# Optimization experiments

Measured on AMD Instinct MI355X. Metric: run time of the kernel, lower is better.

## Reference

```python
import jax, jax.numpy as jnp
from jax import lax
import numpy as np

B, L, FEAT, EXTRA, K1 = 128, 128, 36, 12, 3
EMB, H, A, T_OUT = 6, 1024, 256, 24
CONV_OUT = FEAT - 2 * (K1 - 1)  # 32


def _conv1d(x, w):
    return lax.conv_general_dilated(x, w, (1,), 'VALID', dimension_numbers=('NCW', 'OIW', 'NCW'))


def _lstm(x_t, h, c, Wih, Whh, b):
    g = x_t @ Wih.T + h @ Whh.T + b
    i, f, gg, o = jnp.split(g, 4, axis=-1)
    c = jax.nn.sigmoid(f) * c + jax.nn.sigmoid(i) * jnp.tanh(gg)
    h = jax.nn.sigmoid(o) * jnp.tanh(c)
    return h, c


def setup_inputs():
    key = jax.random.key(0)
    ks = jax.random.split(key, 20)
    s = 0.05
    r = lambda k, sh: jax.random.normal(k, sh, jnp.float32) * s
    return {
        'x': jax.random.normal(ks[0], (B, L, FEAT + EXTRA), jnp.float32),
        'conv1_w': r(ks[1], (L, L, K1)), 'conv1_b': r(ks[2], (L,)),
        'conv2_w': r(ks[3], (L, L, K1)), 'conv2_b': r(ks[4], (L,)),
        'lin3_w': r(ks[5], (EMB, CONV_OUT)), 'lin3_b': r(ks[6], (EMB,)),
        'enc_Wih': r(ks[7], (4 * H, EMB + EXTRA)), 'enc_Whh': r(ks[8], (4 * H, H)), 'enc_b': r(ks[9], (4 * H,)),
        'attn_Wq': r(ks[10], (A, H)), 'attn_Wk': r(ks[11], (A, H)), 'attn_Wv': r(ks[12], (1, A)),
        'dec_Wih': r(ks[13], (4 * H, 2 * H)), 'dec_Whh': r(ks[14], (4 * H, H)), 'dec_b': r(ks[15], (4 * H,)),
        'out_w': r(ks[16], (1, H)), 'out_b': r(ks[17], (1,)),
    }


def reference(x, conv1_w, conv1_b, conv2_w, conv2_b, lin3_w, lin3_b,
              enc_Wih, enc_Whh, enc_b, attn_Wq, attn_Wk, attn_Wv,
              dec_Wih, dec_Whh, dec_b, out_w, out_b):
    # CNN feature extractor over the dense (short-interval) features
    dense = x[:, :, :FEAT]                                   # (B, L, 36)
    h1 = jax.nn.softplus(_conv1d(dense, conv1_w) + conv1_b[None, :, None])
    h2 = jax.nn.relu(_conv1d(h1, conv2_w) + conv2_b[None, :, None])  # (B, L, 32)
    lin = jnp.einsum('blf,ef->ble', h2, lin3_w) + lin3_b     # (B, L, EMB)
    lstm_in = jnp.concatenate([lin, x[:, :, FEAT:]], axis=2)  # (B, L, EMB+EXTRA)

    # LSTM encoder
    def enc_step(carry, xt):
        h, c = carry
        h, c = _lstm(xt, h, c, enc_Wih, enc_Whh, enc_b)
        return (h, c), h
    z = jnp.zeros((B, H), jnp.float32)
    (h, c), outs = lax.scan(enc_step, (z, z), lstm_in.transpose(1, 0, 2))
    enc_out = outs.transpose(1, 0, 2)                        # (B, L, H)
    s = enc_out[:, -1]

    # fixed-size key buffer; original appends s_t each step (lengths 128..151)
    M = L - 1 + T_OUT
    buf0 = jnp.zeros((B, M, H), jnp.float32).at[:, :L - 1].set(enc_out[:, :-1])
    pos = jnp.arange(M)

    def dec_step(carry, t):
        h, c, s, buf = carry
        buf = lax.dynamic_update_slice(buf, s[:, None, :], (0, L - 1 + t, 0))
        mask = (pos <= L - 1 + t).astype(buf.dtype)
        q = jnp.stack([h, c], axis=1)                        # (B, 2, H)
        qp = q @ attn_Wq.T                                   # (B, 2, A)
        kp = buf @ attn_Wk.T                                 # (B, M, A)
        feats = jnp.tanh(qp[:, :, None, :] + kp[:, None, :, :])  # (B, 2, M, A)
        scores = jnp.einsum('bnma,a->bnm', feats, attn_Wv[0])
        # original: softmax over dim=1 (query axis); mask keys post-softmax
        w = jax.nn.softmax(scores, axis=1) * mask[None, None, :]
        ctx = jnp.einsum('bnm,bmh->bnh', w, buf).reshape(B, 2 * H)
        h, c = _lstm(ctx, h, c, dec_Wih, dec_Whh, dec_b)
        y = (h @ out_w.T + out_b)[:, 0]
        return (h, c, h, buf), y

    _, ys = lax.scan(dec_step, (h, c, s, buf0), jnp.arange(T_OUT))
    return ys.T                                              # (B, T_OUT)
```

## Files before the change

### kernel.cpp

```cpp
#include <hip/hip_runtime.h>
#include <math.h>


#define NB 128
#define NL 128
#define NH 1024
#define NA 256
#define NT 24
#define NM 151
#define ENCB 128

typedef __attribute__((ext_vector_type(8))) short bf16x8;
typedef __attribute__((ext_vector_type(8))) short s16x8;
typedef __attribute__((ext_vector_type(4))) float f32x4;

#define MFMA(a, b, acc) __builtin_amdgcn_mfma_f32_16x16x32_bf16(a, b, acc, 0, 0, 0)

#define I16_SCALE 32767.0f
#define I16_INV   (1.0f / 32767.0f)

__device__ __forceinline__ float sig_f(float x) {
  return 1.0f / (1.0f + __expf(-x));
}
__device__ __forceinline__ float tanh_f(float x) {
  x = fminf(9.0f, fmaxf(-9.0f, x));
  float e = __expf(2.0f * x);
  return (e - 1.0f) / (e + 1.0f);
}
__device__ __forceinline__ unsigned short f2bf(float f) {
  unsigned int u = __float_as_uint(f);
  u = (u + 0x7FFFu + ((u >> 16) & 1u)) >> 16;
  return (unsigned short)u;
}
__device__ __forceinline__ float bf2f(unsigned short u) {
  return __uint_as_float(((unsigned int)u) << 16);
}
__device__ __forceinline__ short f2i16(float f) {
  return (short)__float2int_rn(f * I16_SCALE);
}

__device__ __forceinline__ void ast8(unsigned short* p, unsigned short a,
                                     unsigned short b, unsigned short cc,
                                     unsigned short d) {
  unsigned long long u = (unsigned long long)a | ((unsigned long long)b << 16) |
                         ((unsigned long long)cc << 32) |
                         ((unsigned long long)d << 48);
  __hip_atomic_store((unsigned long long*)p, u, __ATOMIC_RELAXED,
                     __HIP_MEMORY_SCOPE_AGENT);
}

#define LLCLD(dst, ptr) \
  asm volatile("global_load_dwordx4 %0, %1, off sc0 sc1" \
               : "=v"(dst) : "v"(ptr))

#define WAITC(n)                                              \
  asm volatile("s_waitcnt vmcnt(" #n ")" ::: "memory");       \
  __builtin_amdgcn_sched_barrier(0)

__device__ __forceinline__ void gbar(unsigned int* bar, int t) {
  __syncthreads();
  if (threadIdx.x == 0) {
    unsigned int* cnt = bar + t * 32;
    __hip_atomic_fetch_add(cnt, 1u, __ATOMIC_RELAXED,
                           __HIP_MEMORY_SCOPE_AGENT);
    while (__hip_atomic_load(cnt, __ATOMIC_RELAXED,
                             __HIP_MEMORY_SCOPE_AGENT) < (unsigned)ENCB)
      __builtin_amdgcn_s_sleep(2);
  }
  __syncthreads();
}

__global__ __launch_bounds__(128) void conv_front(
    const float* __restrict__ x,
    const float* __restrict__ w1, const float* __restrict__ b1,
    const float* __restrict__ w2, const float* __restrict__ b2,
    const float* __restrict__ w3, const float* __restrict__ b3,
    float* __restrict__ lstm_in)
{
  int b = blockIdx.x;
  int t = threadIdx.x;
  __shared__ float d[128][36];
  __shared__ float h1[128][34];
  __shared__ float h2[128][32];

  const float* xr = x + (size_t)(b * NL + t) * 48;
  #pragma unroll
  for (int f = 0; f < 36; ++f) d[t][f] = xr[f];
  __syncthreads();

  float acc[34];
  {
    float bias = b1[t];
    #pragma unroll
    for (int w = 0; w < 34; ++w) acc[w] = bias;
  }
  const float* wr = w1 + t * 384;
  for (int ci = 0; ci < 128; ++ci) {
    float row[36];
    #pragma unroll
    for (int f = 0; f < 36; ++f) row[f] = d[ci][f];
    float wa = wr[ci * 3 + 0], wb = wr[ci * 3 + 1], wc = wr[ci * 3 + 2];
    #pragma unroll
    for (int w = 0; w < 34; ++w)
      acc[w] += row[w] * wa + row[w + 1] * wb + row[w + 2] * wc;
  }
  #pragma unroll
  for (int w = 0; w < 34; ++w) {
    float z = acc[w];
    h1[t][w] = (z > 20.0f) ? z : log1pf(__expf(z));
  }
  __syncthreads();

  float acc2[32];
  {
    float bias = b2[t];
    #pragma unroll
    for (int w = 0; w < 32; ++w) acc2[w] = bias;
  }
  const float* wr2 = w2 + t * 384;
// ... 87 lines not shown
  int t2 = o >> 6;
  int l15 = lane & 15, q = lane >> 4;
  int grow = (l15 >> 2) * 1024 + t2 * 4 + (l15 & 3);
  unsigned short hv[8], lv[8];
  #pragma unroll
  for (int j = 0; j < 8; ++j) {
    int k = q * 8 + j;
    float v = (k < 18) ? wih[(size_t)grow * 18 + k] : 0.0f;
    hv[j] = f2bf(v);
    lv[j] = f2bf(v - bf2f(hv[j]));
  }
  size_t e = (size_t)o * 8;
  *(ushort4*)(hi + e) = make_ushort4(hv[0], hv[1], hv[2], hv[3]);
  *(ushort4*)(hi + e + 4) = make_ushort4(hv[4], hv[5], hv[6], hv[7]);
  *(ushort4*)(lo + e) = make_ushort4(lv[0], lv[1], lv[2], lv[3]);
  *(ushort4*)(lo + e + 4) = make_ushort4(lv[4], lv[5], lv[6], lv[7]);
}

__global__ void frag_xs(const float* __restrict__ lstm_in,
                        unsigned short* __restrict__ hi,
                        unsigned short* __restrict__ lo)
{
  int o = blockIdx.x * 256 + threadIdx.x;
  if (o >= 65536) return;
  int lane = o & 63;
  int btile = (o >> 6) & 7;
  int t = o >> 9;
  int l15 = lane & 15, q = lane >> 4;
  int b = btile * 16 + l15;
  unsigned short hv[8], lv[8];
  #pragma unroll
  for (int j = 0; j < 8; ++j) {
    int k = q * 8 + j;
    float v = (k < 18) ? lstm_in[(size_t)(b * NL + t) * 18 + k] : 0.0f;
    hv[j] = f2bf(v);
    lv[j] = f2bf(v - bf2f(hv[j]));
  }
  size_t e = (size_t)o * 8;
  *(ushort4*)(hi + e) = make_ushort4(hv[0], hv[1], hv[2], hv[3]);
  *(ushort4*)(hi + e + 4) = make_ushort4(hv[4], hv[5], hv[6], hv[7]);
  *(ushort4*)(lo + e) = make_ushort4(lv[0], lv[1], lv[2], lv[3]);
  *(ushort4*)(lo + e + 4) = make_ushort4(lv[4], lv[5], lv[6], lv[7]);
}

__global__ void init_all(float* __restrict__ c,
                         unsigned short* __restrict__ hhi0,
                         unsigned short* __restrict__ hlo0,
                         float* __restrict__ out,
                         unsigned int* __restrict__ bar) {
  int i = blockIdx.x * 256 + threadIdx.x;
  if (i < NB * NH) { c[i] = 0.0f; hhi0[i] = 0; hlo0[i] = 0; }
  if (i < NB * NT) out[i] = 0.0f;
  if (i < 8192) bar[i] = 0;
}

__global__ __launch_bounds__(512) void enc_all(
    unsigned short* __restrict__ hfA_hi, unsigned short* __restrict__ hfA_lo,
    unsigned short* __restrict__ hfB_hi, unsigned short* __restrict__ hfB_lo,
    const unsigned short* __restrict__ Wf_hi,
    const unsigned short* __restrict__ Wf_lo,
    const unsigned short* __restrict__ Wxf_hi,
    const unsigned short* __restrict__ Wxf_lo,
    const unsigned short* __restrict__ xsf_hi,
    const unsigned short* __restrict__ xsf_lo,
    const float* __restrict__ encb,
    float* __restrict__ c,
    short* __restrict__ buf,
    unsigned int* __restrict__ bar)
{
  __shared__ __align__(16) unsigned short SWh[32768];
  __shared__ __align__(16) unsigned short SWl[32768];
  __shared__ __align__(16) unsigned short SXh[1024];
  __shared__ __align__(16) unsigned short SXl[1024];
  __shared__ float G[128][33];

  int tid = threadIdx.x, bx = blockIdx.x;
  int w8 = tid >> 6, lane = tid & 63;
  int l15 = lane & 15, q4 = (lane >> 4) * 4;
  int ab = w8;
  int lane8 = lane * 8;
  size_t abl8 = (size_t)ab * 512 + lane8;

  {
    const unsigned short* gh = Wf_hi + (size_t)(bx * 2) * 16384;
    const unsigned short* gl = Wf_lo + (size_t)(bx * 2) * 16384;
    for (int i = tid * 8; i < 32768; i += 4096) {
      *(bf16x8*)(SWh + i) = *(const bf16x8*)(gh + i);
      *(bf16x8*)(SWl + i) = *(const bf16x8*)(gl + i);
    }
    if (tid < 128) {
      *(bf16x8*)(SXh + tid * 8) =
          *(const bf16x8*)(Wxf_hi + (size_t)(bx * 2) * 512 + tid * 8);
      *(bf16x8*)(SXl + tid * 8) =
          *(const bf16x8*)(Wxf_lo + (size_t)(bx * 2) * 512 + tid * 8);
    }
  }

  int eb = tid >> 1;
  int lt = tid & 1;
  int ekc = bx * 8 + lt * 4;
  float bias[4][4];
  #pragma unroll
  for (int q = 0; q < 4; ++q)
    #pragma unroll
    for (int j = 0; j < 4; ++j)
      bias[q][j] = encb[q * NH + ekc + j];
// ... 82 lines not shown
        float cn = sig_f(gate[1]) * cp[j] + sig_f(gate[0]) * tanh_f(gate[2]);
        float hn = sig_f(gate[3]) * tanh_f(cn);
        cp[j] = cn; rh[j] = hn;
      }
      unsigned short hh[4], hl[4];
      short hq[4];
      #pragma unroll
      for (int j = 0; j < 4; ++j) {
        hh[j] = f2bf(rh[j]);
        hl[j] = f2bf(rh[j] - bf2f(hh[j]));
        hq[j] = f2i16(rh[j]);
      }
      ast8(hoh + efo, hh[0], hh[1], hh[2], hh[3]);
      ast8(hol + efo, hl[0], hl[1], hl[2], hl[3]);
      *(short4*)(buf + (size_t)(eb * NM + t) * NH + ekc) =
          make_short4(hq[0], hq[1], hq[2], hq[3]);
    }
    if (t < NL - 1) gbar(bar, t);
  }
  if (tid < 256)
    *(float4*)(c + (size_t)eb * NH + ekc) = creg;
#undef COMP1
#undef ISSUE
}

__global__ __launch_bounds__(256) void dec_prep(
    const unsigned short* __restrict__ hf_hi,
    const unsigned short* __restrict__ hf_lo,
    const float* __restrict__ c,
    unsigned short* __restrict__ qhi, unsigned short* __restrict__ qlo)
{
  int b = blockIdx.x;
  int j4 = threadIdx.x * 4;
  int ki = j4 >> 5, qq = (j4 >> 3) & 3, j8 = j4 & 7;
  size_t fh = (size_t)ki * 4096 + (b >> 4) * 512 + ((b & 15) + 16 * qq) * 8 + j8;
  ushort4 hv = *(const ushort4*)(hf_hi + fh);
  ushort4 lv = *(const ushort4*)(hf_lo + fh);
  float4 cv = *(const float4*)(c + (size_t)b * NH + j4);
  unsigned short ch[4], cl[4];
  float cf[4] = {cv.x, cv.y, cv.z, cv.w};
  #pragma unroll
  for (int k = 0; k < 4; ++k) {
    ch[k] = f2bf(cf[k]); cl[k] = f2bf(cf[k] - bf2f(ch[k]));
  }
  int rt = (2 * b) >> 4;
  int rl = ((2 * b) & 15) + 16 * qq;
  size_t fq = (size_t)ki * 8192 + rt * 512 + rl * 8 + j8;
  *(ushort4*)(qhi + fq) = hv;
  *(ushort4*)(qlo + fq) = lv;
  *(ushort4*)(qhi + fq + 8) = make_ushort4(ch[0], ch[1], ch[2], ch[3]);
  *(ushort4*)(qlo + fq + 8) = make_ushort4(cl[0], cl[1], cl[2], cl[3]);
}

__global__ __launch_bounds__(128) void gemm_qk(
    const unsigned short* __restrict__ Ahi, const unsigned short* __restrict__ Alo,
    const unsigned short* __restrict__ Bhi, const unsigned short* __restrict__ Blo,
    float* __restrict__ C)
{
  int tid = threadIdx.x;
  int w = tid >> 6, lane = tid & 63;
  int l15 = lane & 15, q4 = (lane >> 4) * 4;
  int mtile = blockIdx.x;
  int ntile = blockIdx.y * 2 + w;

  const unsigned short* Ah = Ahi + (size_t)mtile * 512 + lane * 8;
  const unsigned short* Al = Alo + (size_t)mtile * 512 + lane * 8;
  const unsigned short* Bh = Bhi + (size_t)ntile * 16384 + lane * 8;
  const unsigned short* Bl = Blo + (size_t)ntile * 16384 + lane * 8;
  f32x4 acc = {0, 0, 0, 0};
  for (int ki = 0; ki < 32; ++ki) {
    size_t ao = (size_t)ki * 8192;
    size_t bo = (size_t)ki * 512;
    bf16x8 ah = *(const bf16x8*)(Ah + ao);
    bf16x8 al = *(const bf16x8*)(Al + ao);
    bf16x8 bh = *(const bf16x8*)(Bh + bo);
    bf16x8 bl = *(const bf16x8*)(Bl + bo);
    acc = MFMA(ah, bh, acc);
    acc = MFMA(al, bh, acc);
    acc = MFMA(ah, bl, acc);
  }
  #pragma unroll
  for (int r = 0; r < 4; ++r)
    C[(size_t)(mtile * 16 + q4 + r) * 512 + ntile * 16 + l15] = acc[r];
}

__global__ __launch_bounds__(256) void gemm_kp(
    const short* __restrict__ A,
    const unsigned short* __restrict__ Bhi,
    const unsigned short* __restrict__ Blo,
    unsigned short* __restrict__ C)
{
  int tid = threadIdx.x;
  int w = tid >> 6, lane = tid & 63;
  int l15 = lane & 15, q8 = (lane >> 4) * 8, q4 = (lane >> 4) * 4;
  size_t m0 = (size_t)blockIdx.x * 64;
  int n0 = blockIdx.y * 64 + w * 16;
  int ntile = 16 + blockIdx.y * 4 + w;

  const unsigned short* Bh = Bhi + (size_t)ntile * 16384 + lane * 8;
  const unsigned short* Bl = Blo + (size_t)ntile * 16384 + lane * 8;
  f32x4 acc[4] = {{0,0,0,0},{0,0,0,0},{0,0,0,0},{0,0,0,0}};
  for (int ki = 0; ki < 32; ++ki) {
    int ko = ki * 32 + q8;
    size_t bo = (size_t)ki * 512;
    bf16x8 bh = *(const bf16x8*)(Bh + bo);
    bf16x8 bl = *(const bf16x8*)(Bl + bo);
    #pragma unroll
    for (int i = 0; i < 4; ++i) {
      s16x8 av = *(const s16x8*)(A + (m0 + 16 * i + l15) * (size_t)NH + ko);
      bf16x8 ah;
      #pragma unroll
      for (int k = 0; k < 8; ++k)
        ah[k] = (short)f2bf((float)av[k] * I16_INV);
      acc[i] = MFMA(ah, bh, acc[i]);
      acc[i] = MFMA(ah, bl, acc[i]);
    }
  }
  #pragma unroll
  for (int i = 0; i < 4; ++i)
    #pragma unroll
    for (int r = 0; r < 4; ++r)
      C[(m0 + 16 * i + q4 + r) * NA + n0 + l15] = f2bf(acc[i][r]);
}

__global__ __launch_bounds__(256) void attn_kernel(
    const float* __restrict__ qkout,
    unsigned short* __restrict__ kp,
    const short* __restrict__ buf,
    const float* __restrict__ Wv,
    unsigned short* __restrict__ Xfhi,
    unsigned short* __restrict__ Xflo,
    int t)
{
  int b = blockIdx.x;
  int tid = threadIdx.x;
  int Mt = NL + t;
  __shared__ float sWv[256], q0[256], q1[256], kNew[256];
  __shared__ float sc[2][NM + 1];
  __shared__ float w0s[NM + 1], w1s[NM + 1];
  sWv[tid] = Wv[tid];
  q0[tid] = qkout[(size_t)(2 * b) * 512 + tid];
  q1[tid] = qkout[(size_t)(2 * b + 1) * 512 + tid];
  float kn = qkout[(size_t)(2 * b) * 512 + 256 + tid];
  kNew[tid] = kn;
  kp[((size_t)(b * NM) + (NL - 1 + t)) * NA + tid] = f2bf(kn);
  __syncthreads();

  for (int idx = tid; idx < 2 * Mt; idx += 256) {
    int m = idx >> 1, n = idx & 1;
    const float* q = n ? q1 : q0;
    float s = 0.0f;
    if (m == Mt - 1) {
      for (int a = 0; a < NA; ++a) s += tanh_f(q[a] + kNew[a]) * sWv[a];
    } else {
      const unsigned short* kpr = kp + ((size_t)(b * NM) + m) * NA;
      for (int a = 0; a < NA; a += 4) {
        ushort4 kv = *(const ushort4*)(kpr + a);
        s += tanh_f(q[a + 0] + bf2f(kv.x)) * sWv[a + 0];
        s += tanh_f(q[a + 1] + bf2f(kv.y)) * sWv[a + 1];
        s += tanh_f(q[a + 2] + bf2f(kv.z)) * sWv[a + 2];
        s += tanh_f(q[a + 3] + bf2f(kv.w)) * sWv[a + 3];
      }
    }
    sc[n][m] = s;
  }
  __syncthreads();
  for (int m = tid; m < Mt; m += 256) {
    float s0 = sc[0][m], s1 = sc[1][m];
    float mx = fmaxf(s0, s1);
    float e0 = __expf(s0 - mx), e1 = __expf(s1 - mx);
    float inv = 1.0f / (e0 + e1);
    w0s[m] = e0 * inv;
    w1s[m] = e1 * inv;
  }
  __syncthreads();

  float4 a0 = {0, 0, 0, 0}, a1 = {0, 0, 0, 0};
  const short* bb = buf + ((size_t)b * NM) * NH + tid * 4;
  for (int m = 0; m < Mt; ++m) {
    short4 v = *(const short4*)(bb + (size_t)m * NH);
    float vx = (float)v.x * I16_INV, vy = (float)v.y * I16_INV;
    float vz = (float)v.z * I16_INV, vw = (float)v.w * I16_INV;
    float w0 = w0s[m], w1 = w1s[m];
    a0.x += vx * w0; a0.y += vy * w0; a0.z += vz * w0; a0.w += vw * w0;
    a1.x += vx * w1; a1.y += vy * w1; a1.z += vz * w1; a1.w += vw * w1;
  }
  float v0[4] = {a0.x, a0.y, a0.z, a0.w};
  float v1[4] = {a1.x, a1.y, a1.z, a1.w};
  unsigned short h0[4], l0[4], h1v[4], l1v[4];
  #pragma unroll
  for (int k = 0; k < 4; ++k) {
    h0[k] = f2bf(v0[k]); l0[k] = f2bf(v0[k] - bf2f(h0[k]));
    h1v[k] = f2bf(v1[k]); l1v[k] = f2bf(v1[k] - bf2f(h1v[k]));
  }
  int k0 = tid * 4;
  size_t fo0 = (size_t)(k0 >> 5) * 4096 + (b >> 4) * 512 +
               ((b & 15) + 16 * ((k0 >> 3) & 3)) * 8 + (k0 & 7);
  int k1 = 1024 + tid * 4;
  size_t fo1 = (size_t)(k1 >> 5) * 4096 + (b >> 4) * 512 +
               ((b & 15) + 16 * ((k1 >> 3) & 3)) * 8 + (k1 & 7);
  *(ushort4*)(Xfhi + fo0) = make_ushort4(h0[0], h0[1], h0[2], h0[3]);
  *(ushort4*)(Xflo + fo0) = make_ushort4(l0[0], l0[1], l0[2], l0[3]);
  *(ushort4*)(Xfhi + fo1) = make_ushort4(h1v[0], h1v[1], h1v[2], h1v[3]);
  *(ushort4*)(Xflo + fo1) = make_ushort4(l1v[0], l1v[1], l1v[2], l1v[3]);
}

__global__ __launch_bounds__(512) void dec_step(
    const unsigned short* __restrict__ Xfhi,
    const unsigned short* __restrict__ Xflo,
    const unsigned short* __restrict__ qin_hi,
    const unsigned short* __restrict__ qin_lo,
    unsigned short* __restrict__ qout_hi,
    unsigned short* __restrict__ qout_lo,
    const unsigned short* __restrict__ Wdxf_hi,
    const unsigned short* __restrict__ Wdxf_lo,
    const unsigned short* __restrict__ Wdhf_hi,
    const unsigned short* __restrict__ Wdhf_lo,
    const float* __restrict__ decb,
    float* __restrict__ c,
    short* __restrict__ buf,
    const float* __restrict__ out_w, const float* __restrict__ out_b,
    float* __restrict__ out, int t)
{
  __shared__ float G[2][128][17];
  int tid = threadIdx.x;
  int w8 = tid >> 6, lane = tid & 63;
  int grp = w8 >> 2, wm = w8 & 3;
  int l15 = lane & 15, q4 = (lane >> 4) * 4;
  int bx = blockIdx.x;

  f32x4 a00 = {0,0,0,0}, a10 = {0,0,0,0};

  {
    const unsigned short* Wh = Wdxf_hi + (size_t)bx * 32768 + lane * 8;
    const unsigned short* Wl = Wdxf_lo + (size_t)bx * 32768 + lane * 8;
    const unsigned short* X0h = Xfhi + (size_t)(2 * wm) * 512 + lane * 8;
    const unsigned short* X1h = Xfhi + (size_t)(2 * wm + 1) * 512 + lane * 8;
    const unsigned short* X0l = Xflo + (size_t)(2 * wm) * 512 + lane * 8;
    const unsigned short* X1l = Xflo + (size_t)(2 * wm + 1) * 512 + lane * 8;
    int klo = grp ? 48 : 0;
    int khi = grp ? 64 : 48;
    for (int ki = klo; ki < khi; ++ki) {
      size_t ao = (size_t)ki * 4096;
      size_t bo = (size_t)ki * 512;
      bf16x8 x0h = *(const bf16x8*)(X0h + ao);
      bf16x8 x0l = *(const bf16x8*)(X0l + ao);
      bf16x8 x1h = *(const bf16x8*)(X1h + ao);
      bf16x8 x1l = *(const bf16x8*)(X1l + ao);
      bf16x8 yh = *(const bf16x8*)(Wh + bo);
      bf16x8 yl = *(const bf16x8*)(Wl + bo);
      a00 = MFMA(x0h, yh, a00); a00 = MFMA(x0l, yh, a00); a00 = MFMA(x0h, yl, a00);
      a10 = MFMA(x1h, yh, a10); a10 = MFMA(x1l, yh, a10); a10 = MFMA(x1h, yl, a10);
    }
  }
  if (grp) {
    int qt0 = 4 * wm + (l15 >> 3);
    int ln = 2 * (l15 & 7) + 16 * (lane >> 4);
    const unsigned short* A0h = qin_hi + (size_t)qt0 * 512 + ln * 8;
    const unsigned short* A0l = qin_lo + (size_t)qt0 * 512 + ln * 8;
    const unsigned short* A1h = qin_hi + (size_t)(qt0 + 2) * 512 + ln * 8;
    const unsigned short* A1l = qin_lo + (size_t)(qt0 + 2) * 512 + ln * 8;
    const unsigned short* Bh = Wdhf_hi + (size_t)bx * 16384 + lane * 8;
    const unsigned short* Bl = Wdhf_lo + (size_t)bx * 16384 + lane * 8;
    for (int ki = 0; ki < 32; ++ki) {
      size_t ao = (size_t)ki * 8192;
      size_t bo = (size_t)ki * 512;
      bf16x8 x0h = *(const bf16x8*)(A0h + ao);
      bf16x8 x0l = *(const bf16x8*)(A0l + ao);
      bf16x8 x1h = *(const bf16x8*)(A1h + ao);
      bf16x8 x1l = *(const bf16x8*)(A1l + ao);
      bf16x8 yh = *(const bf16x8*)(Bh + bo);
      bf16x8 yl = *(const bf16x8*)(Bl + bo);
      a00 = MFMA(x0h, yh, a00); a00 = MFMA(x0l, yh, a00); a00 = MFMA(x0h, yl, a00);
      a10 = MFMA(x1h, yh, a10); a10 = MFMA(x1l, yh, a10); a10 = MFMA(x1h, yl, a10);
    }
  }
  #pragma unroll
  for (int r = 0; r < 4; ++r) {
    G[grp][32 * wm + q4 + r][l15]      = a00[r];
    G[grp][32 * wm + 16 + q4 + r][l15] = a10[r];
  }
  __syncthreads();

  if (tid < 128) {
    int b = tid;
    int kc = bx * 4;
    float4 cold = *(const float4*)(c + (size_t)b * NH + kc);
    float rc[4], rh[4];
    #pragma unroll
    for (int j = 0; j < 4; ++j) {
      float gate[4];
      #pragma unroll
      for (int q = 0; q < 4; ++q) {
        int gi = q * 4 + j;
        gate[q] = G[0][b][gi] + G[1][b][gi] + decb[q * NH + kc + j];
      }
      float co = (&cold.x)[j];
      float cn = sig_f(gate[1]) * co + sig_f(gate[0]) * tanh_f(gate[2]);
      float hn = sig_f(gate[3]) * tanh_f(cn);
      rc[j] = cn; rh[j] = hn;
    }
    *(float4*)(c + (size_t)b * NH + kc) = make_float4(rc[0], rc[1], rc[2], rc[3]);

    float py = 0.0f;
    #pragma unroll
    for (int j = 0; j < 4; ++j) py += rh[j] * out_w[kc + j];
    if (bx == 0) py += out_b[0];
    atomicAdd(&out[b * NT + t], py);

    if (t < NT - 1) {
      unsigned short hh[4], hl[4], ch[4], cl[4];
      short hq[4];
      #pragma unroll
      for (int j = 0; j < 4; ++j) {
        hh[j] = f2bf(rh[j]); hl[j] = f2bf(rh[j] - bf2f(hh[j]));
        ch[j] = f2bf(rc[j]); cl[j] = f2bf(rc[j] - bf2f(ch[j]));
        hq[j] = f2i16(rh[j]);
      }
      *(short4*)(buf + (size_t)(b * NM + NL + t) * NH + kc) =
          make_short4(hq[0], hq[1], hq[2], hq[3]);
      int ki = kc >> 5, qq = (kc >> 3) & 3, j8 = kc & 7;
      int rt = (2 * b) >> 4;
      int rl = ((2 * b) & 15) + 16 * qq;
      size_t fq = (size_t)ki * 8192 + rt * 512 + rl * 8 + j8;
      *(ushort4*)(qout_hi + fq) = make_ushort4(hh[0], hh[1], hh[2], hh[3]);
      *(ushort4*)(qout_lo + fq) = make_ushort4(hl[0], hl[1], hl[2], hl[3]);
      *(ushort4*)(qout_hi + fq + 8) = make_ushort4(ch[0], ch[1], ch[2], ch[3]);
      *(ushort4*)(qout_lo + fq + 8) = make_ushort4(cl[0], cl[1], cl[2], cl[3]);
    }
  }
}

extern "C" void kernel_launch(void* const* d_in, const int* in_sizes, int n_in,
                              void* d_out, int out_size, void* d_ws, size_t ws_size,
                              hipStream_t stream) {
  const float* x       = (const float*)d_in[0];
  const float* conv1_w = (const float*)d_in[1];
  const float* conv1_b = (const float*)d_in[2];
  const float* conv2_w = (const float*)d_in[3];
  const float* conv2_b = (const float*)d_in[4];
  const float* lin3_w  = (const float*)d_in[5];
  const float* lin3_b  = (const float*)d_in[6];
  const float* enc_Wih = (const float*)d_in[7];
  const float* enc_Whh = (const float*)d_in[8];
  const float* enc_b   = (const float*)d_in[9];
  const float* attn_Wq = (const float*)d_in[10];
  const float* attn_Wk = (const float*)d_in[11];
  const float* attn_Wv = (const float*)d_in[12];
  const float* dec_Wih = (const float*)d_in[13];
  const float* dec_Whh = (const float*)d_in[14];
  const float* dec_b   = (const float*)d_in[15];
  const float* out_w   = (const float*)d_in[16];
  const float* out_b   = (const float*)d_in[17];
  float* out = (float*)d_out;

  unsigned short* W = (unsigned short*)d_ws;
  short*          buf    = (short*)W;
  unsigned short* kp     = W + (size_t)19791872;
  unsigned short* qA_hi  = kp + 4947968;
  unsigned short* qA_lo  = qA_hi + 262144;
  unsigned short* qB_hi  = qA_lo + 262144;
  unsigned short* qB_lo  = qB_hi + 262144;
  unsigned short* Xf_hi  = qB_lo + 262144;
  unsigned short* Xf_lo  = Xf_hi + 262144;
  unsigned short* Wqkf_hi = Xf_lo + 262144;
  unsigned short* Wqkf_lo = Wqkf_hi + 524288;
  unsigned short* Wdhf_hi = Wqkf_lo + 524288;
  unsigned short* Wdhf_lo = Wdhf_hi + 4194304;
  unsigned short* Wdxf_hi = Wdhf_lo + 4194304;
  unsigned short* Wdxf_lo = Wdxf_hi + 8388608;
  float* c     = (float*)(Wdxf_lo + 8388608);
  float* qkout = c + 131072;
  unsigned short* hfA_hi = Wdxf_hi;
  unsigned short* hfA_lo = Wdxf_hi + 131072;
  unsigned short* hfB_hi = Wdxf_hi + 262144;
  unsigned short* hfB_lo = Wdxf_hi + 393216;
  unsigned short* xsf_hi = Wdxf_hi + 524288;
  unsigned short* xsf_lo = xsf_hi + 524288;
  unsigned short* Wxf_hi = xsf_lo + 524288;
  unsigned short* Wxf_lo = Wxf_hi + 131072;
  float* lstm_in = (float*)Wdxf_lo;
  unsigned int* bar = (unsigned int*)(Wdxf_lo + 1048576);

  init_all<<<512, 256, 0, stream>>>(c, hfA_hi, hfA_lo, out, bar);
  conv_front<<<NB, 128, 0, stream>>>(x, conv1_w, conv1_b, conv2_w, conv2_b,
                                     lin3_w, lin3_b, lstm_in);
  frag_xs<<<256, 256, 0, stream>>>(lstm_in, xsf_hi, xsf_lo);
  frag_wx4<<<64, 256, 0, stream>>>(enc_Wih, Wxf_hi, Wxf_lo);
  frag_w4<<<2048, 256, 0, stream>>>(enc_Whh, 1024, 5, Wdhf_hi, Wdhf_lo, 524288);
  frag_wqk<<<256, 256, 0, stream>>>(attn_Wq, attn_Wk, Wqkf_hi, Wqkf_lo);

  {
    void* ea[] = {
      (void*)&hfA_hi, (void*)&hfA_lo, (void*)&hfB_hi, (void*)&hfB_lo,
      (void*)&Wdhf_hi, (void*)&Wdhf_lo, (void*)&Wxf_hi, (void*)&Wxf_lo,
      (void*)&xsf_hi, (void*)&xsf_lo, (void*)&enc_b, (void*)&c, (void*)&buf,
      (void*)&bar
    };
    hipLaunchCooperativeKernel((void*)enc_all, dim3(ENCB), dim3(512), ea, 0,
                               stream);
  }

  dec_prep<<<NB, 256, 0, stream>>>(hfA_hi, hfA_lo, c, qA_hi, qA_lo);
  gemm_kp<<<dim3(302, 4), 256, 0, stream>>>(buf, Wqkf_hi, Wqkf_lo, kp);

  frag_w4<<<4096, 256, 0, stream>>>(dec_Wih, 2048, 6, Wdxf_hi, Wdxf_lo, 1048576);
  frag_w4<<<2048, 256, 0, stream>>>(dec_Whh, 1024, 5, Wdhf_hi, Wdhf_lo, 524288);

  for (int t = 0; t < NT; ++t) {
    const unsigned short* qih = (t & 1) ? qB_hi : qA_hi;
    const unsigned short* qil = (t & 1) ? qB_lo : qA_lo;
    unsigned short* qoh = (t & 1) ? qA_hi : qB_hi;
    unsigned short* qol = (t & 1) ? qA_lo : qB_lo;
    gemm_qk<<<dim3(16, 16), 128, 0, stream>>>(qih, qil, Wqkf_hi, Wqkf_lo, qkout);
    attn_kernel<<<NB, 256, 0, stream>>>(qkout, kp, buf, attn_Wv, Xf_hi, Xf_lo, t);
    dec_step<<<256, 512, 0, stream>>>(Xf_hi, Xf_lo, qih, qil, qoh, qol,
                                      Wdxf_hi, Wdxf_lo, Wdhf_hi, Wdhf_lo,
                                      dec_b, c, buf, out_w, out_b, out, t);
  }
}
```

Baseline: 4.432 ms.

## Fuse decoder loop into one persistent cooperative kernel with grid barriers

Replaces the 72 per-step launches (q/k GEMM, attention, LSTM step) with a single cooperative persistent kernel of 128 blocks that loops over decoder steps and separates phases with atomic grid barriers. Each block keeps its slice of the recurrent weights resident in LDS and holds cell state and biases in registers. Activation loads are software-pipelined with cache-bypassing loads. This removes launch overhead and reloading of the recurrent weights each step, at the cost of three grid-wide barriers per step, fewer blocks (128 instead of 256) for the LSTM GEMM, and more LDS per block.

New measurement: 10.12 ms. 128% more time.

```diff
diff --git a/kernel.cpp b/kernel.cpp
--- a/kernel.cpp
+++ b/kernel.cpp
@@ -9,6 +9,7 @@
 #define NT 24
 #define NM 151
 #define ENCB 128
+#define DECB 128
 
 typedef __attribute__((ext_vector_type(8))) short bf16x8;
 typedef __attribute__((ext_vector_type(8))) short s16x8;
@@ -48,9 +49,19 @@
   __hip_atomic_store((unsigned long long*)p, u, __ATOMIC_RELAXED,
                      __HIP_MEMORY_SCOPE_AGENT);
 }
+__device__ __forceinline__ void astf(float* p, float v) {
+  __hip_atomic_store((unsigned int*)p, __float_as_uint(v), __ATOMIC_RELAXED,
+                     __HIP_MEMORY_SCOPE_AGENT);
+}
 
 #define LLCLD(dst, ptr) \
   asm volatile("global_load_dwordx4 %0, %1, off sc0 sc1" \
+               : "=v"(dst) : "v"(ptr))
+#define LLCLD4(dst, ptr) \
+  asm volatile("global_load_dword %0, %1, off sc0 sc1" \
+               : "=v"(dst) : "v"(ptr))
+#define LLCLD8(dst, ptr) \
+  asm volatile("global_load_dwordx2 %0, %1, off sc0 sc1" \
                : "=v"(dst) : "v"(ptr))
 
 #define WAITC(n)                                              \
@@ -65,6 +76,17 @@
                            __HIP_MEMORY_SCOPE_AGENT);
     while (__hip_atomic_load(cnt, __ATOMIC_RELAXED,
                              __HIP_MEMORY_SCOPE_AGENT) < (unsigned)ENCB)
+      __builtin_amdgcn_s_sleep(2);
+  }
+  __syncthreads();
+}
+__device__ __forceinline__ void gbar2(unsigned int* cell) {
+  __syncthreads();
+  if (threadIdx.x == 0) {
+    __hip_atomic_fetch_add(cell, 1u, __ATOMIC_RELAXED,
+                           __HIP_MEMORY_SCOPE_AGENT);
+    while (__hip_atomic_load(cell, __ATOMIC_RELAXED,
+                             __HIP_MEMORY_SCOPE_AGENT) < (unsigned)DECB)
       __builtin_amdgcn_s_sleep(2);
   }
   __syncthreads();
@@ -258,6 +280,10 @@
   if (i < NB * NH) { c[i] = 0.0f; hhi0[i] = 0; hlo0[i] = 0; }
   if (i < NB * NT) out[i] = 0.0f;
   if (i < 8192) bar[i] = 0;
+}
+
+__global__ void zero_dbar(unsigned int* __restrict__ dbar) {
+  dbar[threadIdx.x] = 0;
 }
 
 __global__ __launch_bounds__(512) void enc_all(
@@ -446,38 +472,6 @@
   *(ushort4*)(qlo + fq + 8) = make_ushort4(cl[0], cl[1], cl[2], cl[3]);
 }
 
-__global__ __launch_bounds__(128) void gemm_qk(
-    const unsigned short* __restrict__ Ahi, const unsigned short* __restrict__ Alo,
-    const unsigned short* __restrict__ Bhi, const unsigned short* __restrict__ Blo,
-    float* __restrict__ C)
-{
-  int tid = threadIdx.x;
-  int w = tid >> 6, lane = tid & 63;
-  int l15 = lane & 15, q4 = (lane >> 4) * 4;
-  int mtile = blockIdx.x;
-  int ntile = blockIdx.y * 2 + w;
-
-  const unsigned short* Ah = Ahi + (size_t)mtile * 512 + lane * 8;
-  const unsigned short* Al = Alo + (size_t)mtile * 512 + lane * 8;
-  const unsigned short* Bh = Bhi + (size_t)ntile * 16384 + lane * 8;
-  const unsigned short* Bl = Blo + (size_t)ntile * 16384 + lane * 8;
-  f32x4 acc = {0, 0, 0, 0};
-  for (int ki = 0; ki < 32; ++ki) {
-    size_t ao = (size_t)ki * 8192;
-    size_t bo = (size_t)ki * 512;
-    bf16x8 ah = *(const bf16x8*)(Ah + ao);
-    bf16x8 al = *(const bf16x8*)(Al + ao);
-    bf16x8 bh = *(const bf16x8*)(Bh + bo);
-    bf16x8 bl = *(const bf16x8*)(Bl + bo);
-    acc = MFMA(ah, bh, acc);
-    acc = MFMA(al, bh, acc);
-    acc = MFMA(ah, bl, acc);
-  }
-  #pragma unroll
-  for (int r = 0; r < 4; ++r)
-    C[(size_t)(mtile * 16 + q4 + r) * 512 + ntile * 16 + l15] = acc[r];
-}
-
 __global__ __launch_bounds__(256) void gemm_kp(
     const short* __restrict__ A,
     const unsigned short* __restrict__ Bhi,
@@ -517,212 +511,310 @@
       C[(m0 + 16 * i + q4 + r) * NA + n0 + l15] = f2bf(acc[i][r]);
 }
 
-__global__ __launch_bounds__(256) void attn_kernel(
-    const float* __restrict__ qkout,
-    unsigned short* __restrict__ kp,
-    const short* __restrict__ buf,
-    const float* __restrict__ Wv,
-    unsigned short* __restrict__ Xfhi,
-    unsigned short* __restrict__ Xflo,
-    int t)
+__global__ __launch_bounds__(512) void dec_all(
+    unsigned short* __restrict__ Xfh, unsigned short* __restrict__ Xfl,
+    unsigned short* __restrict__ qAh, unsigned short* __restrict__ qAl,
+    unsigned short* __restrict__ qBh, unsigned short* __restrict__ qBl,
+    const unsigned short* __restrict__ Wqh, const unsigned short* __restrict__ Wql,
+    const unsigned short* __restrict__ WdxHg, const unsigned short* __restrict__ WdxLg,
+    const unsigned short* __restrict__ WdhHg, const unsigned short* __restrict__ WdhLg,
+    const float* __restrict__ decb, const float* __restrict__ cin,
+    short* __restrict__ buf, unsigned short* __restrict__ kp,
+    float* __restrict__ qkout, const float* __restrict__ Wv,
+    const float* __restrict__ out_w, const float* __restrict__ out_b,
+    float* __restrict__ out, unsigned int* __restrict__ dbar)
 {
-  int b = blockIdx.x;
-  int tid = threadIdx.x;
-  int Mt = NL + t;
-  __shared__ float sWv[256], q0[256], q1[256], kNew[256];
-  __shared__ float sc[2][NM + 1];
+  __shared__ __align__(16) unsigned short SDh[32768];
+  __shared__ __align__(16) unsigned short SDl[32768];
+  __shared__ float G[128][33];
+  __shared__ float sWv[256], q0s[256], q1s[256], kNs[256];
+  __shared__ float sc2[2][NM + 1];
   __shared__ float w0s[NM + 1], w1s[NM + 1];
-  sWv[tid] = Wv[tid];
-  q0[tid] = qkout[(size_t)(2 * b) * 512 + tid];
-  q1[tid] = qkout[(size_t)(2 * b + 1) * 512 + tid];
-  float kn = qkout[(size_t)(2 * b) * 512 + 256 + tid];
-  kNew[tid] = kn;
-  kp[((size_t)(b * NM) + (NL - 1 + t)) * NA + tid] = f2bf(kn);
+
+  int tid = threadIdx.x, bx = blockIdx.x;
+  int w8 = tid >> 6, lane = tid & 63;
+  int l15 = lane & 15, q4 = (lane >> 4) * 4;
+  int ab = w8;
+  int lane8 = lane * 8;
+  int b = bx;
+
+  {
+    const unsigned short* gh = WdhHg + (size_t)bx * 32768;
+    const unsigned short* gl = WdhLg + (size_t)bx * 32768;
+    for (int i = tid * 8; i < 32768; i += 4096) {
+      *(bf16x8*)(SDh + i) = *(const bf16x8*)(gh + i);
+      *(bf16x8*)(SDl + i) = *(const bf16x8*)(gl + i);
+    }
+  }
+  if (tid < 256) sWv[tid] = Wv[tid];
+
+  int eb = tid >> 1, lt = tid & 1;
+  int ekc = bx * 8 + lt * 4;
+  float dbias[4][4], ow4[4];
+  float4 creg = make_float4(0.f, 0.f, 0.f, 0.f);
+  if (tid < 256) {
+    #pragma unroll
+    for (int q = 0; q < 4; ++q)
+      #pragma unroll
+      for (int j = 0; j < 4; ++j)
+        dbias[q][j] = decb[q * NH + ekc + j];
+    #pragma unroll
+    for (int j = 0; j < 4; ++j) ow4[j] = out_w[ekc + j];
+    creg = *(const float4*)(cin + (size_t)eb * NH + ekc);
+  }
+  float ob = out_b[0];
+  int eki = ekc >> 5, eqq = (ekc >> 3) & 3, ej8 = ekc & 7;
+  int ert = (2 * eb) >> 4;
+  int erl = ((2 * eb) & 15) + 16 * eqq;
+  size_t efq = (size_t)eki * 8192 + ert * 512 + erl * 8 + ej8;
   __syncthreads();
 
-  for (int idx = tid; idx < 2 * Mt; idx += 256) {
-    int m = idx >> 1, n = idx & 1;
-    const float* q = n ? q1 : q0;
-    float s = 0.0f;
-    if (m == Mt - 1) {
-      for (int a = 0; a < NA; ++a) s += tanh_f(q[a] + kNew[a]) * sWv[a];
-    } else {
-      const unsigned short* kpr = kp + ((size_t)(b * NM) + m) * NA;
-      for (int a = 0; a < NA; a += 4) {
-        ushort4 kv = *(const ushort4*)(kpr + a);
-        s += tanh_f(q[a + 0] + bf2f(kv.x)) * sWv[a + 0];
-        s += tanh_f(q[a + 1] + bf2f(kv.y)) * sWv[a + 1];
-        s += tanh_f(q[a + 2] + bf2f(kv.z)) * sWv[a + 2];
-        s += tanh_f(q[a + 3] + bf2f(kv.w)) * sWv[a + 3];
-      }
-    }
-    sc[n][m] = s;
-  }
-  __syncthreads();
-  for (int m = tid; m < Mt; m += 256) {
-    float s0 = sc[0][m], s1 = sc[1][m];
-    float mx = fmaxf(s0, s1);
-    float e0 = __expf(s0 - mx), e1 = __expf(s1 - mx);
-    float inv = 1.0f / (e0 + e1);
-    w0s[m] = e0 * inv;
-    w1s[m] = e1 * inv;
-  }
-  __syncthreads();
-
-  float4 a0 = {0, 0, 0, 0}, a1 = {0, 0, 0, 0};
-  const short* bb = buf + ((size_t)b * NM) * NH + tid * 4;
-  for (int m = 0; m < Mt; ++m) {
-    short4 v = *(const short4*)(bb + (size_t)m * NH);
-    float vx = (float)v.x * I16_INV, vy = (float)v.y * I16_INV;
-    float vz = (float)v.z * I16_INV, vw = (float)v.w * I16_INV;
-    float w0 = w0s[m], w1 = w1s[m];
-    a0.x += vx * w0; a0.y += vy * w0; a0.z += vz * w0; a0.w += vw * w0;
-    a1.x += vx * w1; a1.y += vy * w1; a1.z += vz * w1; a1.w += vw * w1;
-  }
-  float v0[4] = {a0.x, a0.y, a0.z, a0.w};
-  float v1[4] = {a1.x, a1.y, a1.z, a1.w};
-  unsigned short h0[4], l0[4], h1v[4], l1v[4];
-  #pragma unroll
-  for (int k = 0; k < 4; ++k) {
-    h0[k] = f2bf(v0[k]); l0[k] = f2bf(v0[k] - bf2f(h0[k]));
-    h1v[k] = f2bf(v1[k]); l1v[k] = f2bf(v1[k] - bf2f(h1v[k]));
-  }
-  int k0 = tid * 4;
-  size_t fo0 = (size_t)(k0 >> 5) * 4096 + (b >> 4) * 512 +
-               ((b & 15) + 16 * ((k0 >> 3) & 3)) * 8 + (k0 & 7);
-  int k1 = 1024 + tid * 4;
-  size_t fo1 = (size_t)(k1 >> 5) * 4096 + (b >> 4) * 512 +
-               ((b & 15) + 16 * ((k1 >> 3) & 3)) * 8 + (k1 & 7);
-  *(ushort4*)(Xfhi + fo0) = make_ushort4(h0[0], h0[1], h0[2], h0[3]);
-  *(ushort4*)(Xflo + fo0) = make_ushort4(l0[0], l0[1], l0[2], l0[3]);
-  *(ushort4*)(Xfhi + fo1) = make_ushort4(h1v[0], h1v[1], h1v[2], h1v[3]);
-  *(ushort4*)(Xflo + fo1) = make_ushort4(l1v[0], l1v[1], l1v[2], l1v[3]);
-}
-
-__global__ __launch_bounds__(512) void dec_step(
-    const unsigned short* __restrict__ Xfhi,
-    const unsigned short* __restrict__ Xflo,
-    const unsigned short* __restrict__ qin_hi,
-    const unsigned short* __restrict__ qin_lo,
-    unsigned short* __restrict__ qout_hi,
-    unsigned short* __restrict__ qout_lo,
-    const unsigned short* __restrict__ Wdxf_hi,
-    const unsigned short* __restrict__ Wdxf_lo,
-    const unsigned short* __restrict__ Wdhf_hi,
-    const unsigned short* __restrict__ Wdhf_lo,
-    const float* __restrict__ decb,
-    float* __restrict__ c,
-    short* __restrict__ buf,
-    const float* __restrict__ out_w, const float* __restrict__ out_b,
-    float* __restrict__ out, int t)
-{
-  __shared__ float G[2][128][17];
-  int tid = threadIdx.x;
-  int w8 = tid >> 6, lane = tid & 63;
-  int grp = w8 >> 2, wm = w8 & 3;
-  int l15 = lane & 15, q4 = (lane >> 4) * 4;
-  int bx = blockIdx.x;
-
-  f32x4 a00 = {0,0,0,0}, a10 = {0,0,0,0};
-
-  {
-    const unsigned short* Wh = Wdxf_hi + (size_t)bx * 32768 + lane * 8;
-    const unsigned short* Wl = Wdxf_lo + (size_t)bx * 32768 + lane * 8;
-    const unsigned short* X0h = Xfhi + (size_t)(2 * wm) * 512 + lane * 8;
-    const unsigned short* X1h = Xfhi + (size_t)(2 * wm + 1) * 512 + lane * 8;
-    const unsigned short* X0l = Xflo + (size_t)(2 * wm) * 512 + lane * 8;
-    const unsigned short* X1l = Xflo + (size_t)(2 * wm + 1) * 512 + lane * 8;
-    int klo = grp ? 48 : 0;
-    int khi = grp ? 64 : 48;
-    for (int ki = klo; ki < khi; ++ki) {
-      size_t ao = (size_t)ki * 4096;
-      size_t bo = (size_t)ki * 512;
-      bf16x8 x0h = *(const bf16x8*)(X0h + ao);
-      bf16x8 x0l = *(const bf16x8*)(X0l + ao);
-      bf16x8 x1h = *(const bf16x8*)(X1h + ao);
-      bf16x8 x1l = *(const bf16x8*)(X1l + ao);
-      bf16x8 yh = *(const bf16x8*)(Wh + bo);
-      bf16x8 yl = *(const bf16x8*)(Wl + bo);
-      a00 = MFMA(x0h, yh, a00); a00 = MFMA(x0l, yh, a00); a00 = MFMA(x0h, yl, a00);
-      a10 = MFMA(x1h, yh, a10); a10 = MFMA(x1l, yh, a10); a10 = MFMA(x1h, yl, a10);
-    }
-  }
-  if (grp) {
-    int qt0 = 4 * wm + (l15 >> 3);
-    int ln = 2 * (l15 & 7) + 16 * (lane >> 4);
-    const unsigned short* A0h = qin_hi + (size_t)qt0 * 512 + ln * 8;
-    const unsigned short* A0l = qin_lo + (size_t)qt0 * 512 + ln * 8;
-    const unsigned short* A1h = qin_hi + (size_t)(qt0 + 2) * 512 + ln * 8;
-    const unsigned short* A1l = qin_lo + (size_t)(qt0 + 2) * 512 + ln * 8;
-    const unsigned short* Bh = Wdhf_hi + (size_t)bx * 16384 + lane * 8;
-    const unsigned short* Bl = Wdhf_lo + (size_t)bx * 16384 + lane * 8;
-    for (int ki = 0; ki < 32; ++ki) {
-      size_t ao = (size_t)ki * 8192;
-      size_t bo = (size_t)ki * 512;
-      bf16x8 x0h = *(const bf16x8*)(A0h + ao);
-      bf16x8 x0l = *(const bf16x8*)(A0l + ao);
-      bf16x8 x1h = *(const bf16x8*)(A1h + ao);
-      bf16x8 x1l = *(const bf16x8*)(A1l + ao);
-      bf16x8 yh = *(const bf16x8*)(Bh + bo);
-      bf16x8 yl = *(const bf16x8*)(Bl + bo);
-      a00 = MFMA(x0h, yh, a00); a00 = MFMA(x0l, yh, a00); a00 = MFMA(x0h, yl, a00);
-      a10 = MFMA(x1h, yh, a10); a10 = MFMA(x1l, yh, a10); a10 = MFMA(x1h, yl, a10);
-    }
-  }
-  #pragma unroll
-  for (int r = 0; r < 4; ++r) {
-    G[grp][32 * wm + q4 + r][l15]      = a00[r];
-    G[grp][32 * wm + 16 + q4 + r][l15] = a10[r];
-  }
-  __syncthreads();
-
-  if (tid < 128) {
-    int b = tid;
-    int kc = bx * 4;
-    float4 cold = *(const float4*)(c + (size_t)b * NH + kc);
-    float rc[4], rh[4];
-    #pragma unroll
-    for (int j = 0; j < 4; ++j) {
-      float gate[4];
-      #pragma unroll
-      for (int q = 0; q < 4; ++q) {
-        int gi = q * 4 + j;
-        gate[q] = G[0][b][gi] + G[1][b][gi] + decb[q * NH + kc + j];
-      }
-      float co = (&cold.x)[j];
-      float cn = sig_f(gate[1]) * co + sig_f(gate[0]) * tanh_f(gate[2]);
-      float hn = sig_f(gate[3]) * tanh_f(cn);
-      rc[j] = cn; rh[j] = hn;
-    }
-    *(float4*)(c + (size_t)b * NH + kc) = make_float4(rc[0], rc[1], rc[2], rc[3]);
-
-    float py = 0.0f;
-    #pragma unroll
-    for (int j = 0; j < 4; ++j) py += rh[j] * out_w[kc + j];
-    if (bx == 0) py += out_b[0];
-    atomicAdd(&out[b * NT + t], py);
-
-    if (t < NT - 1) {
-      unsigned short hh[4], hl[4], ch[4], cl[4];
-      short hq[4];
+#define P_ISSUE(P, J, APH, APL, STRIDE)                                     \
+  _Pragma("unroll")                                                         \
+  for (int i_ = 0; i_ < 8; ++i_) {                                          \
+    LLCLD(axh[(P) * 8 + i_], (APH) + (size_t)((J) * 8 + i_) * (STRIDE));    \
+    LLCLD(axl[(P) * 8 + i_], (APL) + (size_t)((J) * 8 + i_) * (STRIDE));    \
+  }
+
+  for (int t = 0; t < NT; ++t) {
+    const unsigned short* qih = (t & 1) ? qBh : qAh;
+    const unsigned short* qil = (t & 1) ? qBl : qAl;
+    unsigned short* qoh = (t & 1) ? qAh : qBh;
+    unsigned short* qol = (t & 1) ? qAl : qBl;
+    int Mt = NL + t;
+
+    if (w8 < 4) {
+      int g = bx * 4 + w8;
+      int mtile = g >> 5, ntile = g & 31;
+      const unsigned short* Ah = qih + (size_t)mtile * 512 + lane8;
+      const unsigned short* Al = qil + (size_t)mtile * 512 + lane8;
+      const unsigned short* Bh = Wqh + (size_t)ntile * 16384 + lane8;
+      const unsigned short* Bl = Wql + (size_t)ntile * 16384 + lane8;
+      f32x4 acc = {0, 0, 0, 0};
+      bf16x8 axh[16], axl[16];
+      P_ISSUE(0, 0, Ah, Al, 8192);
       #pragma unroll
       for (int j = 0; j < 4; ++j) {
-        hh[j] = f2bf(rh[j]); hl[j] = f2bf(rh[j] - bf2f(hh[j]));
-        ch[j] = f2bf(rc[j]); cl[j] = f2bf(rc[j] - bf2f(ch[j]));
-        hq[j] = f2i16(rh[j]);
-      }
-      *(short4*)(buf + (size_t)(b * NM + NL + t) * NH + kc) =
-          make_short4(hq[0], hq[1], hq[2], hq[3]);
-      int ki = kc >> 5, qq = (kc >> 3) & 3, j8 = kc & 7;
-      int rt = (2 * b) >> 4;
-      int rl = ((2 * b) & 15) + 16 * qq;
-      size_t fq = (size_t)ki * 8192 + rt * 512 + rl * 8 + j8;
-      *(ushort4*)(qout_hi + fq) = make_ushort4(hh[0], hh[1], hh[2], hh[3]);
-      *(ushort4*)(qout_lo + fq) = make_ushort4(hl[0], hl[1], hl[2], hl[3]);
-      *(ushort4*)(qout_hi + fq + 8) = make_ushort4(ch[0], ch[1], ch[2], ch[3]);
-      *(ushort4*)(qout_lo + fq + 8) = make_ushort4(cl[0], cl[1], cl[2], cl[3]);
-    }
-  }
+        if (j < 3) { P_ISSUE((j + 1) & 1, j + 1, Ah, Al, 8192); }
+        if (j < 3) { WAITC(16); } else { WAITC(0); }
+        #pragma unroll
+        for (int i_ = 0; i_ < 8; ++i_) {
+          size_t bo = (size_t)(j * 8 + i_) * 512;
+          bf16x8 bh = *(const bf16x8*)(Bh + bo);
+          bf16x8 bl = *(const bf16x8*)(Bl + bo);
+          bf16x8 xh_ = axh[(j & 1) * 8 + i_];
+          bf16x8 xl_ = axl[(j & 1) * 8 + i_];
+          acc = MFMA(xh_, bh, acc);
+          acc = MFMA(xl_, bh, acc);
+          acc = MFMA(xh_, bl, acc);
+        }
+      }
+      #pragma unroll
+      for (int r = 0; r < 4; ++r)
+        astf(qkout + (size_t)(mtile * 16 + q4 + r) * 512 + ntile * 16 + l15,
+             acc[r]);
+    }
+    gbar2(dbar + t * 3 + 0);
+
+    if (tid < 256) {
+      unsigned int u0, u1, u2;
+      LLCLD4(u0, (const float*)qkout + (size_t)(2 * b) * 512 + tid);
+      LLCLD4(u1, (const float*)qkout + (size_t)(2 * b + 1) * 512 + tid);
+      LLCLD4(u2, (const float*)qkout + (size_t)(2 * b) * 512 + 256 + tid);
+      WAITC(0);
+      q0s[tid] = __uint_as_float(u0);
+      q1s[tid] = __uint_as_float(u1);
+      float kn = __uint_as_float(u2);
+      kNs[tid] = kn;
+      if (t < NT - 1)
+        kp[((size_t)(b * NM) + (NL - 1 + t)) * NA + tid] = f2bf(kn);
+    }
+    __syncthreads();
+
+    for (int idx = tid; idx < 2 * Mt; idx += 512) {
+      int m = idx >> 1, n = idx & 1;
+      const float* q = n ? q1s : q0s;
+      float s = 0.0f;
+      if (m == Mt - 1) {
+        for (int a = 0; a < NA; ++a) s += tanh_f(q[a] + kNs[a]) * sWv[a];
+      } else {
+        const unsigned short* kpr = kp + ((size_t)(b * NM) + m) * NA;
+        for (int a = 0; a < NA; a += 4) {
+          ushort4 kv = *(const ushort4*)(kpr + a);
+          s += tanh_f(q[a + 0] + bf2f(kv.x)) * sWv[a + 0];
+          s += tanh_f(q[a + 1] + bf2f(kv.y)) * sWv[a + 1];
+          s += tanh_f(q[a + 2] + bf2f(kv.z)) * sWv[a + 2];
+          s += tanh_f(q[a + 3] + bf2f(kv.w)) * sWv[a + 3];
+        }
+      }
+      sc2[n][m] = s;
+    }
+    __syncthreads();
+    for (int m = tid; m < Mt; m += 512) {
+      float s0 = sc2[0][m], s1 = sc2[1][m];
+      float mx = fmaxf(s0, s1);
+      float e0 = __expf(s0 - mx), e1 = __expf(s1 - mx);
+      float inv = 1.0f / (e0 + e1);
+      w0s[m] = e0 * inv;
+      w1s[m] = e1 * inv;
+    }
+    for (int m = Mt + tid; m < NM; m += 512) { w0s[m] = 0.f; w1s[m] = 0.f; }
+    __syncthreads();
+
+    if (tid < 256) {
+      float4 a0 = {0, 0, 0, 0}, a1 = {0, 0, 0, 0};
+      const short* bb = buf + ((size_t)b * NM) * NH + tid * 4;
+      for (int m = 0; m < NL; ++m) {
+        short4 v = *(const short4*)(bb + (size_t)m * NH);
+        float vx = (float)v.x * I16_INV, vy = (float)v.y * I16_INV;
+        float vz = (float)v.z * I16_INV, vw = (float)v.w * I16_INV;
+        float w0 = w0s[m], w1 = w1s[m];
+        a0.x += vx * w0; a0.y += vy * w0; a0.z += vz * w0; a0.w += vw * w0;
+        a1.x += vx * w1; a1.y += vy * w1; a1.z += vz * w1; a1.w += vw * w1;
+      }
+      {
+        union U8 { unsigned long long u; short4 s; } tv[23];
+        #pragma unroll
+        for (int m = 0; m < 23; ++m)
+          LLCLD8(tv[m].u, bb + (size_t)(NL + m) * NH);
+        WAITC(0);
+        #pragma unroll
+        for (int m = 0; m < 23; ++m) {
+          short4 v = tv[m].s;
+          float vx = (float)v.x * I16_INV, vy = (float)v.y * I16_INV;
+          float vz = (float)v.z * I16_INV, vw = (float)v.w * I16_INV;
+          float w0 = w0s[NL + m], w1 = w1s[NL + m];
+          a0.x += vx * w0; a0.y += vy * w0; a0.z += vz * w0; a0.w += vw * w0;
+          a1.x += vx * w1; a1.y += vy * w1; a1.z += vz * w1; a1.w += vw * w1;
+        }
+      }
+      float v0[4] = {a0.x, a0.y, a0.z, a0.w};
+      float v1[4] = {a1.x, a1.y, a1.z, a1.w};
+      unsigned short h0[4], l0[4], h1v[4], l1v[4];
+      #pragma unroll
+      for (int k = 0; k < 4; ++k) {
+        h0[k] = f2bf(v0[k]); l0[k] = f2bf(v0[k] - bf2f(h0[k]));
+        h1v[k] = f2bf(v1[k]); l1v[k] = f2bf(v1[k] - bf2f(h1v[k]));
+      }
+      int k0 = tid * 4;
+      size_t fo0 = (size_t)(k0 >> 5) * 4096 + (b >> 4) * 512 +
+                   ((b & 15) + 16 * ((k0 >> 3) & 3)) * 8 + (k0 & 7);
+      int k1 = 1024 + tid * 4;
+      size_t fo1 = (size_t)(k1 >> 5) * 4096 + (b >> 4) * 512 +
+                   ((b & 15) + 16 * ((k1 >> 3) & 3)) * 8 + (k1 & 7);
+      ast8(Xfh + fo0, h0[0], h0[1], h0[2], h0[3]);
+      ast8(Xfl + fo0, l0[0], l0[1], l0[2], l0[3]);
+      ast8(Xfh + fo1, h1v[0], h1v[1], h1v[2], h1v[3]);
+      ast8(Xfl + fo1, l1v[0], l1v[1], l1v[2], l1v[3]);
+    }
+    gbar2(dbar + t * 3 + 1);
+
+    {
+      f32x4 acc0 = {0,0,0,0}, acc1 = {0,0,0,0};
+      const unsigned short* XAh = Xfh + (size_t)ab * 512 + lane8;
+      const unsigned short* XAl = Xfl + (size_t)ab * 512 + lane8;
+      const unsigned short* WXH = WdxHg + (size_t)bx * 65536 + lane8;
+      const unsigned short* WXL = WdxLg + (size_t)bx * 65536 + lane8;
+      {
+        bf16x8 axh[16], axl[16];
+        P_ISSUE(0, 0, XAh, XAl, 4096);
+        #pragma unroll
+        for (int j = 0; j < 8; ++j) {
+          if (j < 7) { P_ISSUE((j + 1) & 1, j + 1, XAh, XAl, 4096); }
+          if (j < 7) { WAITC(16); } else { WAITC(0); }
+          #pragma unroll
+          for (int i_ = 0; i_ < 8; ++i_) {
+            size_t bo = (size_t)(j * 8 + i_) * 512;
+            bf16x8 bh0 = *(const bf16x8*)(WXH + bo);
+            bf16x8 bl0 = *(const bf16x8*)(WXL + bo);
+            bf16x8 bh1 = *(const bf16x8*)(WXH + 32768 + bo);
+            bf16x8 bl1 = *(const bf16x8*)(WXL + 32768 + bo);
+            bf16x8 xh_ = axh[(j & 1) * 8 + i_];
+            bf16x8 xl_ = axl[(j & 1) * 8 + i_];
+            acc0 = MFMA(xh_, bh0, acc0); acc0 = MFMA(xl_, bh0, acc0);
+            acc0 = MFMA(xh_, bl0, acc0);
+            acc1 = MFMA(xh_, bh1, acc1); acc1 = MFMA(xl_, bh1, acc1);
+            acc1 = MFMA(xh_, bl1, acc1);
+          }
+        }
+      }
+      {
+        const unsigned short* QAh = qih +
+            (size_t)(2 * ab + (l15 >> 3)) * 512 +
+            (2 * (l15 & 7) + 16 * (lane >> 4)) * 8;
+        const unsigned short* QAl = qil +
+            (size_t)(2 * ab + (l15 >> 3)) * 512 +
+            (2 * (l15 & 7) + 16 * (lane >> 4)) * 8;
+        bf16x8 axh[16], axl[16];
+        P_ISSUE(0, 0, QAh, QAl, 8192);
+        #pragma unroll
+        for (int j = 0; j < 4; ++j) {
+          if (j < 3) { P_ISSUE((j + 1) & 1, j + 1, QAh, QAl, 8192); }
+          if (j < 3) { WAITC(16); } else { WAITC(0); }
+          #pragma unroll
+          for (int i_ = 0; i_ < 8; ++i_) {
+            int bo = (j * 8 + i_) * 512 + lane8;
+            bf16x8 bh0 = *(const bf16x8*)(SDh + bo);
+            bf16x8 bl0 = *(const bf16x8*)(SDl + bo);
+            bf16x8 bh1 = *(const bf16x8*)(SDh + 16384 + bo);
+            bf16x8 bl1 = *(const bf16x8*)(SDl + 16384 + bo);
+            bf16x8 xh_ = axh[(j & 1) * 8 + i_];
+            bf16x8 xl_ = axl[(j & 1) * 8 + i_];
+            acc0 = MFMA(xh_, bh0, acc0); acc0 = MFMA(xl_, bh0, acc0);
+            acc0 = MFMA(xh_, bl0, acc0);
+            acc1 = MFMA(xh_, bh1, acc1); acc1 = MFMA(xl_, bh1, acc1);
+            acc1 = MFMA(xh_, bl1, acc1);
+          }
+        }
+      }
+      #pragma unroll
+      for (int r = 0; r < 4; ++r) {
+        G[ab * 16 + q4 + r][l15]      = acc0[r];
+        G[ab * 16 + q4 + r][16 + l15] = acc1[r];
+      }
+    }
+    __syncthreads();
+
+    if (tid < 256) {
+      float rh[4], rc[4];
+      float* cp = &creg.x;
+      #pragma unroll
+      for (int j = 0; j < 4; ++j) {
+        float gate[4];
+        #pragma unroll
+        for (int q = 0; q < 4; ++q)
+          gate[q] = G[eb][lt * 16 + q * 4 + j] + dbias[q][j];
+        float cn = sig_f(gate[1]) * cp[j] + sig_f(gate[0]) * tanh_f(gate[2]);
+        float hn = sig_f(gate[3]) * tanh_f(cn);
+        cp[j] = cn; rc[j] = cn; rh[j] = hn;
+      }
+      float py = 0.0f;
+      #pragma unroll
+      for (int j = 0; j < 4; ++j) py += rh[j] * ow4[j];
+      if (bx == 0 && lt == 0) py += ob;
+      atomicAdd(&out[eb * NT + t], py);
+
+      if (t < NT - 1) {
+        unsigned short hh[4], hl[4], ch[4], cl[4];
+        short hq[4];
+        #pragma unroll
+        for (int j = 0; j < 4; ++j) {
+          hh[j] = f2bf(rh[j]); hl[j] = f2bf(rh[j] - bf2f(hh[j]));
+          ch[j] = f2bf(rc[j]); cl[j] = f2bf(rc[j] - bf2f(ch[j]));
+          hq[j] = f2i16(rh[j]);
+        }
+        ast8((unsigned short*)(buf + (size_t)(eb * NM + NL + t) * NH + ekc),
+             (unsigned short)hq[0], (unsigned short)hq[1],
+             (unsigned short)hq[2], (unsigned short)hq[3]);
+        ast8(qoh + efq, hh[0], hh[1], hh[2], hh[3]);
+        ast8(qol + efq, hl[0], hl[1], hl[2], hl[3]);
+        ast8(qoh + efq + 8, ch[0], ch[1], ch[2], ch[3]);
+        ast8(qol + efq + 8, cl[0], cl[1], cl[2], cl[3]);
+      }
+    }
+    if (t < NT - 1) gbar2(dbar + t * 3 + 2);
+  }
+#undef P_ISSUE
 }
 
 extern "C" void kernel_launch(void* const* d_in, const int* in_sizes, int n_in,
@@ -775,6 +867,7 @@
   unsigned short* Wxf_lo = Wxf_hi + 131072;
   float* lstm_in = (float*)Wdxf_lo;
   unsigned int* bar = (unsigned int*)(Wdxf_lo + 1048576);
+  unsigned int* dbar = (unsigned int*)(kp + (size_t)150 * NA);
 
   init_all<<<512, 256, 0, stream>>>(c, hfA_hi, hfA_lo, out, bar);
   conv_front<<<NB, 128, 0, stream>>>(x, conv1_w, conv1_b, conv2_w, conv2_b,
@@ -797,19 +890,21 @@
 
   dec_prep<<<NB, 256, 0, stream>>>(hfA_hi, hfA_lo, c, qA_hi, qA_lo);
   gemm_kp<<<dim3(302, 4), 256, 0, stream>>>(buf, Wqkf_hi, Wqkf_lo, kp);
+  zero_dbar<<<1, 128, 0, stream>>>(dbar);
 
   frag_w4<<<4096, 256, 0, stream>>>(dec_Wih, 2048, 6, Wdxf_hi, Wdxf_lo, 1048576);
   frag_w4<<<2048, 256, 0, stream>>>(dec_Whh, 1024, 5, Wdhf_hi, Wdhf_lo, 524288);
 
-  for (int t = 0; t < NT; ++t) {
-    const unsigned short* qih = (t & 1) ? qB_hi : qA_hi;
-    const unsigned short* qil = (t & 1) ? qB_lo : qA_lo;
-    unsigned short* qoh = (t & 1) ? qA_hi : qB_hi;
-    unsigned short* qol = (t & 1) ? qA_lo : qB_lo;
-    gemm_qk<<<dim3(16, 16), 128, 0, stream>>>(qih, qil, Wqkf_hi, Wqkf_lo, qkout);
-    attn_kernel<<<NB, 256, 0, stream>>>(qkout, kp, buf, attn_Wv, Xf_hi, Xf_lo, t);
-    dec_step<<<256, 512, 0, stream>>>(Xf_hi, Xf_lo, qih, qil, qoh, qol,
-                                      Wdxf_hi, Wdxf_lo, Wdhf_hi, Wdhf_lo,
-                                      dec_b, c, buf, out_w, out_b, out, t);
-  }
-}
+  {
+    void* da[] = {
+      (void*)&Xf_hi, (void*)&Xf_lo, (void*)&qA_hi, (void*)&qA_lo,
+      (void*)&qB_hi, (void*)&qB_lo, (void*)&Wqkf_hi, (void*)&Wqkf_lo,
+      (void*)&Wdxf_hi, (void*)&Wdxf_lo, (void*)&Wdhf_hi, (void*)&Wdhf_lo,
+      (void*)&dec_b, (void*)&c, (void*)&buf, (void*)&kp, (void*)&qkout,
+      (void*)&attn_Wv, (void*)&out_w, (void*)&out_b, (void*)&out,
+      (void*)&dbar
+    };
+    hipLaunchCooperativeKernel((void*)dec_all, dim3(DECB), dim3(512), da, 0,
+                               stream);
+  }
+}
```
